# Optimization experiments

Hardware: AMD Instinct MI355X
Metric: run time of the kernel (lower is better)

Reference implementation:

```python
import math
import jax, jax.numpy as jnp
import numpy as np

NUM_HEADS = 16
HEAD_DIM = 64
MAX_POS = 2048  # max_position_embeddings


def setup_inputs() -> dict:
    key = jax.random.key(0)
    ks = jax.random.split(key, 8)
    B, S, H = 2, 2048, 1024
    return {
        "hidden_states": jax.random.normal(ks[0], (B, S, H), jnp.float32),
        "Wq": jax.random.normal(ks[1], (H, H), jnp.float32) * 0.02,
        "bq": jax.random.normal(ks[2], (H,), jnp.float32) * 0.02,
        "Wk": jax.random.normal(ks[3], (H, H), jnp.float32) * 0.02,
        "bk": jax.random.normal(ks[4], (H,), jnp.float32) * 0.02,
        "Wv": jax.random.normal(ks[5], (H, H), jnp.float32) * 0.02,
        "bv": jax.random.normal(ks[6], (H,), jnp.float32) * 0.02,
        "dist_emb": jax.random.normal(ks[7], (2 * MAX_POS - 1, HEAD_DIM), jnp.float32) * 0.02,
    }


def reference(hidden_states, Wq, bq, Wk, bk, Wv, bv, dist_emb):
    B, S, H = hidden_states.shape
    nh, hd = NUM_HEADS, HEAD_DIM
    # projections (nn.Linear: x @ W.T + b), split into heads
    q = (hidden_states @ Wq.T + bq).reshape(B, S, nh, hd)
    k = (hidden_states @ Wk.T + bk).reshape(B, S, nh, hd)
    v = (hidden_states @ Wv.T + bv).reshape(B, S, nh, hd)
    scale = 1.0 / math.sqrt(hd)
    scores = jnp.einsum('bqhd,bkhd->bhqk', q, k) * scale  # [B,H,S,S]
    # relative position embeddings: distance = q_pos - k_pos
    pos = jnp.arange(S)
    distance = pos[:, None] - pos[None, :]          # [S,S]
    pe = dist_emb[MAX_POS - 1 + distance]           # [S,S,hd]
    rel_q = jnp.einsum('bqhd,qkd->bhqk', q, pe) * scale
    rel_k = jnp.einsum('bkhd,qkd->bhqk', k, pe) * scale
    scores = scores + rel_q + rel_k
    probs = jax.nn.softmax(scores, axis=-1)         # dropout p=0.0
    ctx = jnp.einsum('bhqk,bkhd->bqhd', probs, v)
    return ctx.reshape(B, S, nh * hd)
```

## Files before the change

### kernel.cpp

```cpp
#include <hip/hip_runtime.h>
#include <hip/hip_bf16.h>

#define NH 16
#define HD 64
#define SEQ 2048
#define HID 1024
#define MAXP 2048
#define ST_R 68

typedef float f32x4 __attribute__((ext_vector_type(4)));
typedef short bf16x8 __attribute__((ext_vector_type(8)));
typedef unsigned short u16;
typedef unsigned short u16x8 __attribute__((ext_vector_type(8)));

__device__ __forceinline__ u16 f2bf_hw(float x) {
  union { __hip_bfloat16 h; u16 u; } v;
  v.h = __float2bfloat16(x);
  return v.u;
}
__device__ __forceinline__ unsigned pk2(float a, float b) {
  return (unsigned)f2bf_hw(a) | ((unsigned)f2bf_hw(b) << 16);
}
__device__ __forceinline__ float bf2f(u16 h) {
  union { unsigned u; float f; } v; v.u = ((unsigned)h) << 16;
  return v.f;
}

#define SWZ(r, c) ((r) * 64 + ((((c) >> 3) ^ ((r) & 7)) << 3) + ((c) & 7))

__device__ __forceinline__ void async_copy16(void* lds, const void* g) {
  __builtin_amdgcn_global_load_lds(
      (const __attribute__((address_space(1))) unsigned int*)g,
      (__attribute__((address_space(3))) unsigned int*)lds, 16, 0, 0);
}
__device__ __forceinline__ void vwait0() { asm volatile("s_waitcnt vmcnt(0)" ::: "memory"); }
__device__ __forceinline__ void lwait0() { asm volatile("s_waitcnt lgkmcnt(0)" ::: "memory"); }

__global__ __launch_bounds__(256) void cvt_f32_bf16(
    const float* __restrict__ src, u16* __restrict__ dst, int n4) {
  int i = blockIdx.x * 256 + threadIdx.x;
  const int stride = gridDim.x * 256;
  for (; i < n4; i += stride) {
    const float4 v = reinterpret_cast<const float4*>(src)[i];
    uint2 d;
    d.x = pk2(v.x, v.y);
    d.y = pk2(v.z, v.w);
    reinterpret_cast<uint2*>(dst)[i] = d;
  }
}

__global__ __launch_bounds__(256) void proj_mfma(
    const u16* __restrict__ Xb, const u16* __restrict__ W0,
    const u16* __restrict__ W1, const u16* __restrict__ W2,
    const float* __restrict__ b0, const float* __restrict__ b1,
    const float* __restrict__ b2,
    u16* __restrict__ O0, u16* __restrict__ O1, u16* __restrict__ O2) {
  __shared__ u16 sA[128 * 64];
  __shared__ u16 sB[128 * 64];
  const int t = threadIdx.x, lane = t & 63, w = t >> 6;
  const int g = lane >> 4, li = lane & 15;
  const int wsel = blockIdx.x >> 3;
  const int n0 = (blockIdx.x & 7) * 128, m0 = blockIdx.y * 128;
  const u16* Wb = wsel == 0 ? W0 : (wsel == 1 ? W1 : W2);
  const float* bias = wsel == 0 ? b0 : (wsel == 1 ? b1 : b2);
  u16* Ob = wsel == 0 ? O0 : (wsel == 1 ? O1 : O2);
  const float oscale = wsel == 0 ? 0.125f : 1.0f;
  const int wr = w >> 1, wc = w & 1;

  f32x4 acc[4][4];
#pragma unroll
  for (int i = 0; i < 4; ++i)
#pragma unroll
    for (int j = 0; j < 4; ++j) acc[i][j] = (f32x4)0.0f;

  for (int k0 = 0; k0 < HID; k0 += 64) {
    __syncthreads();
#pragma unroll
    for (int i = 0; i < 4; ++i) {
      const int idx = (w * 4 + i) * 64 + lane;
      const int row = idx >> 3, sch = (idx & 7) ^ (row & 7);
      async_copy16(&sA[(w * 4 + i) * 512], Xb + (size_t)(m0 + row) * HID + k0 + sch * 8);
      async_copy16(&sB[(w * 4 + i) * 512], Wb + (size_t)(n0 + row) * HID + k0 + sch * 8);
    }
    __syncthreads();
    bf16x8 af[4][2], bfr[4][2];
#pragma unroll
    for (int i = 0; i < 4; ++i)
#pragma unroll
      for (int c = 0; c < 2; ++c)
        af[i][c] = *reinterpret_cast<const bf16x8*>(&sA[SWZ(wr * 64 + 16 * i + li, 32 * c + 8 * g)]);
#pragma unroll
    for (int j = 0; j < 4; ++j)
#pragma unroll
      for (int c = 0; c < 2; ++c)
        bfr[j][c] = *reinterpret_cast<const bf16x8*>(&sB[SWZ(wc * 64 + 16 * j + li, 32 * c + 8 * g)]);
#pragma unroll
    for (int i = 0; i < 4; ++i)
#pragma unroll
      for (int j = 0; j < 4; ++j)
#pragma unroll
        for (int c = 0; c < 2; ++c)
          acc[i][j] = __builtin_amdgcn_mfma_f32_16x16x32_bf16(af[i][c], bfr[j][c], acc[i][j], 0, 0, 0);
  }

#pragma unroll
  for (int j = 0; j < 4; ++j) {
    const float bj = bias[n0 + wc * 64 + 16 * j + li];
#pragma unroll
    for (int i = 0; i < 4; ++i)
#pragma unroll
      for (int r = 0; r < 4; ++r)
        Ob[(size_t)(m0 + wr * 64 + 16 * i + 4 * g + r) * HID + n0 + wc * 64 + 16 * j + li] =
            f2bf_hw((acc[i][j][r] + bj) * oscale);
  }
}

__global__ __launch_bounds__(256) void transpose_v(
    const u16* __restrict__ Vin, u16* __restrict__ Vt) {
  __shared__ u16 tile[64 * 65];
  const int t = threadIdx.x;
  const int s0 = blockIdx.x * 64, h = blockIdx.y, b = blockIdx.z;
  const int r = t >> 2, c0 = (t & 3) * 16;
  const u16* gp = Vin + (size_t)(b * SEQ + s0 + r) * HID + h * HD + c0;
  const u16x8 a0 = *reinterpret_cast<const u16x8*>(gp);
  const u16x8 a1 = *reinterpret_cast<const u16x8*>(gp + 8);
#pragma unroll
  for (int i = 0; i < 8; ++i) { tile[r * 65 + c0 + i] = a0[i]; tile[r * 65 + c0 + 8 + i] = a1[i]; }
  __syncthreads();
  const int d = t >> 2, sc = (t & 3) * 16;
  u16x8 o0, o1;
#pragma unroll
  for (int i = 0; i < 8; ++i) {
    o0[i] = tile[(sc + i) * 65 + d];
    o1[i] = tile[(sc + 8 + i) * 65 + d];
  }
  u16* op = Vt + ((size_t)(b * NH + h) * HD + d) * SEQ + s0 + sc;
  *reinterpret_cast<u16x8*>(op) = o0;
  *reinterpret_cast<u16x8*>(op + 8) = o1;
}

__global__ __launch_bounds__(256, 2) void attn_mfma5(
    const u16* __restrict__ Q, const u16* __restrict__ K,
    const u16* __restrict__ Vt, const u16* __restrict__ E,
    float* __restrict__ out) {
  __shared__ u16 sK0[64 * 64];
  __shared__ u16 sK1[64 * 64];
  __shared__ u16 sV[64 * 64];
  __shared__ u16 sE[128 * 64];
  __shared__ u16 sRq[128 * ST_R];
  __shared__ u16 sRk[128 * ST_R];

  const int t = threadIdx.x;
  const int lane = t & 63, w = t >> 6;
  const int g = lane >> 4, li = lane & 15;
  const int q0 = blockIdx.x * 64;
  const int h = blockIdx.y, b = blockIdx.z;
  const size_t qkbase = (size_t)b * SEQ * HID + (size_t)h * HD;
  const size_t vtbase = (size_t)(b * NH + h) * HD * SEQ;

  bf16x8 qA[2];
#pragma unroll
  for (int c = 0; c < 2; ++c)
    qA[c] = *reinterpret_cast<const bf16x8*>(
        Q + qkbase + (size_t)(q0 + 16 * w + li) * HID + 32 * c + 8 * g);

  f32x4 accO[4];
  float lsum[4];
#pragma unroll
  for (int n = 0; n < 4; ++n) accO[n] = (f32x4)0.0f;
#pragma unroll
  for (int r = 0; r < 4; ++r) lsum[r] = 0.0f;

  const int jb48 = 15 + 16 * w + 4 * g - li;
  const u16* gqp = &sRq[jb48 * ST_R + 16 * w + 4 * g];
  const u16* gkp = &sRk[jb48 * ST_R + li];
  u16* rkw = &sRk[li * ST_R + 16 * w + 4 * g];
  u16* rqw = &sRq[li * ST_R + 16 * w + 4 * g];

  const int sidx2 = w * 2 * 64 + lane;
  const int sidx4 = w * 4 * 64 + lane;

  {
    const int eb0 = 1984 + q0;
#pragma unroll
    for (int i = 0; i < 2; ++i) {
      const int idx = sidx2 + i * 64;
      const int row = idx >> 3, sch = (idx & 7) ^ (row & 7);
      async_copy16(&sK0[(w * 2 + i) * 512], K + qkbase + (size_t)row * HID + sch * 8);
    }
#pragma unroll
    for (int i = 0; i < 4; ++i) {
      const int idx = sidx4 + i * 64;
      const int row = idx >> 3, sch = (idx & 7) ^ (row & 7);
      const int er = min(max(eb0 + row, 0), 2 * MAXP - 2);
      async_copy16(&sE[(w * 4 + i) * 512], E + (size_t)er * HD + sch * 8);
    }
    vwait0();
  }

  for (int k0 = 0; k0 < SEQ; k0 += 64) {
    const int p = (k0 >> 6) & 1;
    u16* kcur = p ? sK1 : sK0;
    u16* knxt = p ? sK0 : sK1;

    __builtin_amdgcn_s_barrier();
#pragma unroll
    for (int i = 0; i < 2; ++i) {
      const int idx = sidx2 + i * 64;
      const int row = idx >> 3, sch = (idx & 7) ^ (row & 7);
      async_copy16(&sV[(w * 2 + i) * 512], Vt + vtbase + (size_t)row * SEQ + k0 + sch * 8);
      async_copy16(&knxt[(w * 2 + i) * 512], K + qkbase + (size_t)(k0 + 64 + row) * HID + sch * 8);
    }

    bf16x8 kA[2];
#pragma unroll
    for (int c = 0; c < 2; ++c)
      kA[c] = *reinterpret_cast<const bf16x8*>(&kcur[SWZ(16 * w + li, 32 * c + 8 * g)]);
    f32x4 aqk[4];
#pragma unroll
    for (int n = 0; n < 4; ++n) {
      aqk[n] = (f32x4)0.0f;
#pragma unroll
      for (int c = 0; c < 2; ++c) {
        const bf16x8 kB = *reinterpret_cast<const bf16x8*>(&kcur[SWZ(16 * n + li, 32 * c + 8 * g)]);
        aqk[n] = __builtin_amdgcn_mfma_f32_16x16x32_bf16(qA[c], kB, aqk[n], 0, 0, 0);
      }
    }
    __builtin_amdgcn_s_setprio(1);
#pragma unroll
    for (int m = 0; m < 8; ++m) {
      bf16x8 eB[2];
#pragma unroll
      for (int c = 0; c < 2; ++c)
        eB[c] = *reinterpret_cast<const bf16x8*>(&sE[SWZ(16 * m + li, 32 * c + 8 * g)]);
      f32x4 ak = (f32x4)0.0f, aq = (f32x4)0.0f;
#pragma unroll
      for (int c = 0; c < 2; ++c) {
        ak = __builtin_amdgcn_mfma_f32_16x16x32_bf16(kA[c], eB[c], ak, 0, 0, 0);
        aq = __builtin_amdgcn_mfma_f32_16x16x32_bf16(qA[c], eB[c], aq, 0, 0, 0);
      }
      uint2 dk, dq;
      dk.x = pk2(ak[0], ak[1]); dk.y = pk2(ak[2], ak[3]);
      dq.x = pk2(aq[0], aq[1]); dq.y = pk2(aq[2], aq[3]);
      *reinterpret_cast<uint2*>(rkw + m * 16 * ST_R) = dk;
      *reinterpret_cast<uint2*>(rqw + m * 16 * ST_R) = dq;
    }
    __builtin_amdgcn_s_setprio(0);

    vwait0();
    lwait0();
    __builtin_amdgcn_s_barrier();

    {
      const int ebn = 1920 + q0 - k0;
#pragma unroll
      for (int i = 0; i < 4; ++i) {
        const int idx = sidx4 + i * 64;
        const int row = idx >> 3, sch = (idx & 7) ^ (row & 7);
        const int er = min(max(ebn + row, 0), 2 * MAXP - 2);
        async_copy16(&sE[(w * 4 + i) * 512], E + (size_t)er * HD + sch * 8);
      }
    }

#pragma unroll
    for (int n = 0; n < 4; ++n)
#pragma unroll
      for (int r = 0; r < 4; ++r) {
        const float relq = bf2f(gqp[(48 + r - 16 * n) * ST_R + r]);
        const float relk = bf2f(gkp[(48 + r - 16 * n) * ST_R + 16 * n]);
        const float pr = __expf(fmaf(relk, 0.125f, aqk[n][r] + relq));
        lsum[r] += pr;
        kcur[SWZ(16 * w + 4 * g + r, 16 * n + li)] = f2bf_hw(pr);
      }

    bf16x8 pA[2];
#pragma unroll
    for (int c = 0; c < 2; ++c)
      pA[c] = *reinterpret_cast<const bf16x8*>(&kcur[SWZ(16 * w + li, 32 * c + 8 * g)]);
#pragma unroll
    for (int n = 0; n < 4; ++n)
#pragma unroll
      for (int c = 0; c < 2; ++c) {
        const bf16x8 vB = *reinterpret_cast<const bf16x8*>(&sV[SWZ(16 * n + li, 32 * c + 8 * g)]);
        accO[n] = __builtin_amdgcn_mfma_f32_16x16x32_bf16(pA[c], vB, accO[n], 0, 0, 0);
      }

    vwait0();
  }

#pragma unroll
  for (int off = 1; off < 16; off <<= 1)
#pragma unroll
    for (int r = 0; r < 4; ++r) lsum[r] += __shfl_xor(lsum[r], off, 16);
#pragma unroll
  for (int r = 0; r < 4; ++r) {
    const float inv = 1.0f / lsum[r];
    const size_t row = (size_t)(b * SEQ + q0 + 16 * w + 4 * g + r) * HID + h * HD;
#pragma unroll
    for (int n = 0; n < 4; ++n) out[row + 16 * n + li] = accO[n][r] * inv;
  }
}

extern "C" void kernel_launch(void* const* d_in, const int* in_sizes, int n_in,
                              void* d_out, int out_size, void* d_ws, size_t ws_size,
                              hipStream_t stream) {
  const float* hs = (const float*)d_in[0];
  const float* Wq = (const float*)d_in[1];
  const float* bq = (const float*)d_in[2];
  const float* Wk = (const float*)d_in[3];
  const float* bk = (const float*)d_in[4];
  const float* Wv = (const float*)d_in[5];
  const float* bv = (const float*)d_in[6];
  const float* de = (const float*)d_in[7];
  float* out = (float*)d_out;

  u16* Xb  = (u16*)d_ws;
  u16* Wqb = Xb + (size_t)4194304;
  u16* Wkb = Wqb + (size_t)1048576;
  u16* Wvb = Wkb + (size_t)1048576;
  u16* Qb  = Wvb + (size_t)1048576;
  u16* Kb  = Qb + (size_t)4194304;
  u16* Vb  = Kb + (size_t)4194304;
  u16* Eb  = Vb + (size_t)4194304;
  u16* Vtb = Xb;

  dim3 blk(256);
  hipLaunchKernelGGL(cvt_f32_bf16, dim3(512), blk, 0, stream, hs, Xb, 1048576);
  hipLaunchKernelGGL(cvt_f32_bf16, dim3(256), blk, 0, stream, Wq, Wqb, 262144);
  hipLaunchKernelGGL(cvt_f32_bf16, dim3(256), blk, 0, stream, Wk, Wkb, 262144);
  hipLaunchKernelGGL(cvt_f32_bf16, dim3(256), blk, 0, stream, Wv, Wvb, 262144);
  hipLaunchKernelGGL(cvt_f32_bf16, dim3(128), blk, 0, stream, de, Eb, 65520);

  hipLaunchKernelGGL(proj_mfma, dim3(24, 32), blk, 0, stream,
                     Xb, Wqb, Wkb, Wvb, bq, bk, bv, Qb, Kb, Vb);
  hipLaunchKernelGGL(transpose_v, dim3(SEQ / 64, NH, 2), blk, 0, stream, Vb, Vtb);
  hipLaunchKernelGGL(attn_mfma5, dim3(SEQ / 64, NH, 2), blk, 0, stream, Qb, Kb, Vtb, Eb, out);
}
```

Measured before the change: 248.2 us.

## Load V fragments from global into registers, use exp2 and MFMA row sums

V fragments are now read from the transposed V buffer straight into registers, which drops the sV shared-memory tile and its LDS reads. The log2(e) factor is folded into the Q projection scale and the relative-key coefficient, so the softmax can use exp2f instead of __expf. The per-row probability sums are computed by an extra MFMA against a vector of bf16 ones rather than scalar adds plus a shuffle reduction. The end-of-iteration vwait0 is removed, so correctness now relies on compiler-inserted waits covering the async K and E prefetches. The direct global V loads may also expose more memory latency per iteration.

```diff
diff --git a/kernel.cpp b/kernel.cpp
--- a/kernel.cpp
+++ b/kernel.cpp
@@ -64,7 +64,7 @@
   const u16* Wb = wsel == 0 ? W0 : (wsel == 1 ? W1 : W2);
   const float* bias = wsel == 0 ? b0 : (wsel == 1 ? b1 : b2);
   u16* Ob = wsel == 0 ? O0 : (wsel == 1 ? O1 : O2);
-  const float oscale = wsel == 0 ? 0.125f : 1.0f;
+  const float oscale = wsel == 0 ? 0.125f * 1.44269504f : 1.0f;
   const int wr = w >> 1, wc = w & 1;
 
   f32x4 acc[4][4];
@@ -139,13 +139,12 @@
   *reinterpret_cast<u16x8*>(op + 8) = o1;
 }
 
-__global__ __launch_bounds__(256, 2) void attn_mfma5(
+__global__ __launch_bounds__(256, 2) void attn_mfma6(
     const u16* __restrict__ Q, const u16* __restrict__ K,
     const u16* __restrict__ Vt, const u16* __restrict__ E,
     float* __restrict__ out) {
   __shared__ u16 sK0[64 * 64];
   __shared__ u16 sK1[64 * 64];
-  __shared__ u16 sV[64 * 64];
   __shared__ u16 sE[128 * 64];
   __shared__ u16 sRq[128 * ST_R];
   __shared__ u16 sRk[128 * ST_R];
@@ -164,12 +163,14 @@
     qA[c] = *reinterpret_cast<const bf16x8*>(
         Q + qkbase + (size_t)(q0 + 16 * w + li) * HID + 32 * c + 8 * g);
 
+  bf16x8 ones;
+#pragma unroll
+  for (int i = 0; i < 8; ++i) ones[i] = (short)0x3F80;
+
   f32x4 accO[4];
-  float lsum[4];
+  f32x4 accX = (f32x4)0.0f;
 #pragma unroll
   for (int n = 0; n < 4; ++n) accO[n] = (f32x4)0.0f;
-#pragma unroll
-  for (int r = 0; r < 4; ++r) lsum[r] = 0.0f;
 
   const int jb48 = 15 + 16 * w + 4 * g - li;
   const u16* gqp = &sRq[jb48 * ST_R + 16 * w + 4 * g];
@@ -208,9 +209,15 @@
     for (int i = 0; i < 2; ++i) {
       const int idx = sidx2 + i * 64;
       const int row = idx >> 3, sch = (idx & 7) ^ (row & 7);
-      async_copy16(&sV[(w * 2 + i) * 512], Vt + vtbase + (size_t)row * SEQ + k0 + sch * 8);
       async_copy16(&knxt[(w * 2 + i) * 512], K + qkbase + (size_t)(k0 + 64 + row) * HID + sch * 8);
     }
+    bf16x8 vf[4][2];
+#pragma unroll
+    for (int n = 0; n < 4; ++n)
+#pragma unroll
+      for (int c = 0; c < 2; ++c)
+        vf[n][c] = *reinterpret_cast<const bf16x8*>(
+            Vt + vtbase + (size_t)(16 * n + li) * SEQ + k0 + 32 * c + 8 * g);
 
     bf16x8 kA[2];
 #pragma unroll
@@ -268,8 +275,7 @@
       for (int r = 0; r < 4; ++r) {
         const float relq = bf2f(gqp[(48 + r - 16 * n) * ST_R + r]);
         const float relk = bf2f(gkp[(48 + r - 16 * n) * ST_R + 16 * n]);
-        const float pr = __expf(fmaf(relk, 0.125f, aqk[n][r] + relq));
-        lsum[r] += pr;
+        const float pr = exp2f(fmaf(relk, 0.125f * 1.44269504f, aqk[n][r] + relq));
         kcur[SWZ(16 * w + 4 * g + r, 16 * n + li)] = f2bf_hw(pr);
       }
 
@@ -280,21 +286,16 @@
 #pragma unroll
     for (int n = 0; n < 4; ++n)
 #pragma unroll
-      for (int c = 0; c < 2; ++c) {
-        const bf16x8 vB = *reinterpret_cast<const bf16x8*>(&sV[SWZ(16 * n + li, 32 * c + 8 * g)]);
-        accO[n] = __builtin_amdgcn_mfma_f32_16x16x32_bf16(pA[c], vB, accO[n], 0, 0, 0);
-      }
-
-    vwait0();
-  }
-
-#pragma unroll
-  for (int off = 1; off < 16; off <<= 1)
-#pragma unroll
-    for (int r = 0; r < 4; ++r) lsum[r] += __shfl_xor(lsum[r], off, 16);
+      for (int c = 0; c < 2; ++c)
+        accO[n] = __builtin_amdgcn_mfma_f32_16x16x32_bf16(pA[c], vf[n][c], accO[n], 0, 0, 0);
+#pragma unroll
+    for (int c = 0; c < 2; ++c)
+      accX = __builtin_amdgcn_mfma_f32_16x16x32_bf16(pA[c], ones, accX, 0, 0, 0);
+  }
+
 #pragma unroll
   for (int r = 0; r < 4; ++r) {
-    const float inv = 1.0f / lsum[r];
+    const float inv = 1.0f / accX[r];
     const size_t row = (size_t)(b * SEQ + q0 + 16 * w + 4 * g + r) * HID + h * HD;
 #pragma unroll
     for (int n = 0; n < 4; ++n) out[row + 16 * n + li] = accO[n][r] * inv;
@@ -334,5 +335,5 @@
   hipLaunchKernelGGL(proj_mfma, dim3(24, 32), blk, 0, stream,
                      Xb, Wqb, Wkb, Wvb, bq, bk, bv, Qb, Kb, Vb);
   hipLaunchKernelGGL(transpose_v, dim3(SEQ / 64, NH, 2), blk, 0, stream, Vb, Vtb);
-  hipLaunchKernelGGL(attn_mfma5, dim3(SEQ / 64, NH, 2), blk, 0, stream, Qb, Kb, Vtb, Eb, out);
-}
+  hipLaunchKernelGGL(attn_mfma6, dim3(SEQ / 64, NH, 2), blk, 0, stream, Qb, Kb, Vtb, Eb, out);
+}
```

Measured after the change: 305.0 us. 22.9% more time.
